# Kernel tuning notes

Hardware: AMD Instinct MI355X
Metric: run time of the kernel (lower is better)

## Reference

```python
import jax, jax.numpy as jnp
import numpy as np

B, C, E = 2, 128, 60000

def conv1(x, W, b):
    # pointwise conv1d: x [B,Cin,E], W [Cout,Cin], b [Cout] -> [B,Cout,E]
    return jnp.einsum('oc,bce->boe', W, x) + b[None, :, None]

def mesh_conv(x, gi, W, b):
    # MeshCNN GeMM conv: x [B,C,E], gi [B,E,4] neighbor edge ids, W [Cout,Cin,5], b [Cout]
    f = jax.vmap(lambda xb, ib: xb[:, ib])(x, gi)  # [B,C,E,4] neighbor gather
    f1, f2, f3, f4 = f[..., 0], f[..., 1], f[..., 2], f[..., 3]
    # symmetric features: [e, a+c, b+d, |a-c|, |b-d|]
    G = jnp.stack([x, f1 + f3, f2 + f4, jnp.abs(f1 - f3), jnp.abs(f2 - f4)], axis=-1)  # [B,C,E,5]
    return jnp.einsum('bces,ocs->boe', G, W) + b[None, :, None]


def setup_inputs() -> dict:
    key = jax.random.key(0)
    ks = jax.random.split(key, 16)
    s = 0.05
    return {
        'x_0': jax.random.normal(ks[0], (B, C, E), jnp.float32),
        'x_1': jax.random.normal(ks[1], (B, C, E), jnp.float32),
        'gemm': jax.random.randint(ks[2], (B, E, 4), 0, E, jnp.int32),
        'Wa_local': jax.random.normal(ks[3], (C, C), jnp.float32) * s,
        'ba_local': jax.random.normal(ks[4], (C,), jnp.float32) * s,
        'Wb_local': jax.random.normal(ks[5], (C, C), jnp.float32) * s,
        'bb_local': jax.random.normal(ks[6], (C,), jnp.float32) * s,
        'Wa_tri': jax.random.normal(ks[7], (C, C, 5), jnp.float32) * s,
        'ba_tri': jax.random.normal(ks[8], (C,), jnp.float32) * s,
        'Wb_tri': jax.random.normal(ks[9], (C, C, 5), jnp.float32) * s,
        'bb_tri': jax.random.normal(ks[10], (C,), jnp.float32) * s,
        'Wa_fuse': jax.random.normal(ks[11], (3, 2 * C), jnp.float32) * s,
        'ba_fuse': jax.random.normal(ks[12], (3,), jnp.float32) * s,
        'Wb_fuse': jax.random.normal(ks[13], (3, 2 * C), jnp.float32) * s,
        'bb_fuse': jax.random.normal(ks[14], (3,), jnp.float32) * s,
    }


def reference(x_0, x_1, gemm, Wa_local, ba_local, Wb_local, bb_local,
              Wa_tri, ba_tri, Wb_tri, bb_tri,
              Wa_fuse, ba_fuse, Wb_fuse, bb_fuse):
    a_local = conv1(x_0, Wa_local, ba_local)              # [B,C,E]
    a_tri = mesh_conv(x_0, gemm, Wa_tri, ba_tri)          # [B,C,E]
    x_a_two = jnp.concatenate([a_local, a_tri], axis=1)   # [B,2C,E]
    b_local = conv1(x_1, Wb_local, bb_local)
    b_tri = mesh_conv(x_1, gemm, Wb_tri, bb_tri)
    x_b_two = jnp.concatenate([b_local, b_tri], axis=1)
    x_a_w = conv1(x_a_two, Wa_fuse, ba_fuse)[:, None]     # [B,1,3,E]
    x_b_w = conv1(x_b_two, Wb_fuse, bb_fuse)[:, None]     # [B,1,3,E]
    return x_a_w + x_b_w
```

## Files before the change

### kernel.cpp

```cpp
#include <hip/hip_runtime.h>
#include <hip/hip_bf16.h>
#include <cstdint>

#define B_ 2
#define C_ 128
#define E_ 60000

typedef unsigned int uint32_;
typedef unsigned short ushort_;
typedef float v2f __attribute__((ext_vector_type(2)));

__device__ __forceinline__ v2f bp2(uint32_ v) {
    v2f r;
    r.x = __uint_as_float(v << 16);
    r.y = __uint_as_float(v & 0xffff0000u);
    return r;
}

__device__ __forceinline__ v2f vabs2(v2f a) {
    v2f r; r.x = fabsf(a.x); r.y = fabsf(a.y); return r;
}

__device__ __forceinline__ ushort_ f2b(float f) {
    union { float f; uint32_ u; } x; x.f = f;
    uint32_ u = x.u + 0x7fffu + ((x.u >> 16) & 1u);
    return (ushort_)(u >> 16);
}

__device__ __forceinline__ float swz_add(float v, const int pat) {
    switch (pat) {
    case 1:  return v + __int_as_float(__builtin_amdgcn_ds_swizzle(__float_as_int(v), 0x041F));
    case 2:  return v + __int_as_float(__builtin_amdgcn_ds_swizzle(__float_as_int(v), 0x081F));
    case 4:  return v + __int_as_float(__builtin_amdgcn_ds_swizzle(__float_as_int(v), 0x101F));
    case 8:  return v + __int_as_float(__builtin_amdgcn_ds_swizzle(__float_as_int(v), 0x201F));
    default: return v + __int_as_float(__builtin_amdgcn_ds_swizzle(__float_as_int(v), 0x401F));
    }
}

__global__ __launch_bounds__(256) void fuse_weights_kernel(
    const float* __restrict__ Wa_local, const float* __restrict__ ba_local,
    const float* __restrict__ Wb_local, const float* __restrict__ bb_local,
    const float* __restrict__ Wa_tri,  const float* __restrict__ ba_tri,
    const float* __restrict__ Wb_tri,  const float* __restrict__ bb_tri,
    const float* __restrict__ Wa_fuse, const float* __restrict__ ba_fuse,
    const float* __restrict__ Wb_fuse, const float* __restrict__ bb_fuse,
    float* __restrict__ Vw, float* __restrict__ cst)
{
    const int lane = threadIdx.x & 63;
    if (blockIdx.x < 15) {
        const int wid   = blockIdx.x * 4 + (threadIdx.x >> 6);
        const int pj    = wid / 10;
        const int chunk = wid % 10;
        const int p = pj / 3, j = pj % 3;
        const int f = chunk * 64 + lane;
        const float* Wf = p ? Wb_fuse : Wa_fuse;
        const float* Wt = p ? Wb_tri  : Wa_tri;
        const float* Wl = p ? Wb_local : Wa_local;
        float a0 = 0.f, a1 = 0.f, a2 = 0.f, a3 = 0.f;
        for (int o = 0; o < C_; o += 4) {
            a0 += Wf[j * 256 + 128 + o]     * Wt[(o)     * 640 + f];
            a1 += Wf[j * 256 + 128 + o + 1] * Wt[(o + 1) * 640 + f];
            a2 += Wf[j * 256 + 128 + o + 2] * Wt[(o + 2) * 640 + f];
            a3 += Wf[j * 256 + 128 + o + 3] * Wt[(o + 3) * 640 + f];
        }
        float acc = (a0 + a1) + (a2 + a3);
        const int s = f % 5, c = f / 5;
        if (s == 0) {
            float b0 = 0.f, b1 = 0.f, b2 = 0.f, b3 = 0.f;
            for (int o = 0; o < C_; o += 4) {
                b0 += Wf[j * 256 + o]     * Wl[(o)     * C_ + c];
                b1 += Wf[j * 256 + o + 1] * Wl[(o + 1) * C_ + c];
                b2 += Wf[j * 256 + o + 2] * Wl[(o + 2) * C_ + c];
                b3 += Wf[j * 256 + o + 3] * Wl[(o + 3) * C_ + c];
            }
            acc += (b0 + b1) + (b2 + b3);
        }
        Vw[(pj * 5 + s) * C_ + c] = acc;
    } else {
        if (threadIdx.x < 3) {
            int j = threadIdx.x;
            float acc = ba_fuse[j] + bb_fuse[j];
            for (int o = 0; o < C_; ++o) {
                acc += Wa_fuse[j * 256 + o]       * ba_local[o]
                     + Wa_fuse[j * 256 + 128 + o] * ba_tri[o]
                     + Wb_fuse[j * 256 + o]       * bb_local[o]
                     + Wb_fuse[j * 256 + 128 + o] * bb_tri[o];
            }
            cst[j] = acc;
        }
    }
}

__global__ __launch_bounds__(256) void transpose_bf16_kernel(
    const float* __restrict__ x0, const float* __restrict__ x1,
    ushort_* __restrict__ x0t, ushort_* __restrict__ x1t)
{
    __shared__ float tile[32][65];
    const int which = blockIdx.z >> 1;
    const int b     = blockIdx.z & 1;
    const float* src = (which ? x1 : x0) + (size_t)b * C_ * E_;
    ushort_*     dst = (which ? x1t : x0t) + (size_t)b * E_ * C_;
    const int e0 = blockIdx.x * 32;
    const int c0 = blockIdx.y * 64;
    const int t  = threadIdx.x;
    {
        const int c  = t >> 2;
        const int e8 = (t & 3) * 8;
        const float* p = src + (size_t)(c0 + c) * E_ + e0 + e8;
        float4 v0 = *(const float4*)p;
        float4 v1 = *(const float4*)(p + 4);
        tile[e8 + 0][c] = v0.x; tile[e8 + 1][c] = v0.y;
        tile[e8 + 2][c] = v0.z; tile[e8 + 3][c] = v0.w;
        tile[e8 + 4][c] = v1.x; tile[e8 + 5][c] = v1.y;
        tile[e8 + 6][c] = v1.z; tile[e8 + 7][c] = v1.w;
    }
    __syncthreads();
    {
        const int e  = t >> 3;
        const int c8 = (t & 7) * 8;
        const float* r = &tile[e][c8];
        uint32_ w0 = (uint32_)f2b(r[0]) | ((uint32_)f2b(r[1]) << 16);
        uint32_ w1 = (uint32_)f2b(r[2]) | ((uint32_)f2b(r[3]) << 16);
        uint32_ w2 = (uint32_)f2b(r[4]) | ((uint32_)f2b(r[5]) << 16);
        uint32_ w3 = (uint32_)f2b(r[6]) | ((uint32_)f2b(r[7]) << 16);
        uint4 w; w.x = w0; w.y = w1; w.z = w2; w.w = w3;
        *(uint4*)(dst + (size_t)(e0 + e) * C_ + c0 + c8) = w;
    }
}

__global__ __launch_bounds__(256, 4) void mesh_fused_kernel(
    const uint32_* __restrict__ x0t, const uint32_* __restrict__ x1t,
    const int* __restrict__ gemm, const float* __restrict__ Vw,
    const float* __restrict__ cst, float* __restrict__ out)
{
    const int lane = threadIdx.x & 63;
    const int wv   = threadIdx.x >> 6;
    const int gw   = blockIdx.x * 4 + wv;
    const int nw   = gridDim.x * 4;

    v2f w[2][3][5];
#pragma unroll
    for (int p = 0; p < 2; ++p)
#pragma unroll
        for (int j = 0; j < 3; ++j)
#pragma unroll
            for (int s = 0; s < 5; ++s)
                w[p][j][s] = *(const v2f*)(Vw + (((p * 3 + j) * 5 + s) << 7) + lane * 2);

    const int  jj     = lane >> 4;
    const bool is0    = (jj == 0), is1 = (jj == 1);
    const bool writer = ((lane & 15) == 0) && (jj < 3);
    const float cj    = is0 ? cst[0] : (is1 ? cst[1] : cst[2]);
    float* obase      = out + (size_t)(jj < 3 ? jj : 2) * E_;

    const int4* g4 = (const int4*)gemm;
    const int npair = (B_ * E_) / 2;

    int4 giA = make_int4(0, 0, 0, 0), giB = giA;
    if (gw < npair) { giA = g4[2 * gw]; giB = g4[2 * gw + 1]; }

    for (int pair = gw; pair < npair; pair += nw) {
        const int nxt = pair + nw;
        const int4 gA = giA, gB = giB;
        if (nxt < npair) { giA = g4[2 * nxt]; giB = g4[2 * nxt + 1]; }

        const int e0 = 2 * pair;
        const int b  = (e0 >= E_) ? 1 : 0;
        const int e  = e0 - (b ? E_ : 0);
        const uint32_* xa = x0t + (size_t)b * (E_ * 64);
        const uint32_* xb = x1t + (size_t)b * (E_ * 64);

        const uint32_ sA = ((uint32_)e << 6) + lane;
        const uint32_ sB = sA + 64;
        const uint32_ oA1 = ((uint32_)gA.x << 6) + lane;
        const uint32_ oA2 = ((uint32_)gA.y << 6) + lane;
        const uint32_ oA3 = ((uint32_)gA.z << 6) + lane;
        const uint32_ oA4 = ((uint32_)gA.w << 6) + lane;
        const uint32_ oB1 = ((uint32_)gB.x << 6) + lane;
        const uint32_ oB2 = ((uint32_)gB.y << 6) + lane;
        const uint32_ oB3 = ((uint32_)gB.z << 6) + lane;
        const uint32_ oB4 = ((uint32_)gB.w << 6) + lane;

        const uint32_ A0 = xa[sA],  A1 = xa[oA1], A2 = xa[oA2], A3 = xa[oA3], A4 = xa[oA4];
        const uint32_ C0 = xb[sA],  C1 = xb[oA1], C2 = xb[oA2], C3 = xb[oA3], C4 = xb[oA4];
        const uint32_ D0 = xa[sB],  D1 = xa[oB1], D2 = xa[oB2], D3 = xa[oB3], D4 = xa[oB4];
        const uint32_ F0 = xb[sB],  F1 = xb[oB1], F2 = xb[oB2], F3 = xb[oB3], F4 = xb[oB4];

        float rA0, rA1, rA2;
        {
            v2f a0 = bp2(A0), a1 = bp2(A1), a2 = bp2(A2), a3 = bp2(A3), a4 = bp2(A4);
            v2f b0 = bp2(C0), b1 = bp2(C1), b2 = bp2(C2), b3 = bp2(C3), b4 = bp2(C4);
            v2f sa1 = a1 + a3, sa2 = a2 + a4;
            v2f da1 = vabs2(a1 - a3), da2 = vabs2(a2 - a4);
            v2f sb1 = b1 + b3, sb2 = b2 + b4;
            v2f db1 = vabs2(b1 - b3), db2 = vabs2(b2 - b4);
            v2f t0 = w[0][0][0] * a0, t1 = w[0][1][0] * a0, t2 = w[0][2][0] * a0;
            t0 += w[0][0][1] * sa1; t1 += w[0][1][1] * sa1; t2 += w[0][2][1] * sa1;
            t0 += w[0][0][2] * sa2; t1 += w[0][1][2] * sa2; t2 += w[0][2][2] * sa2;
            t0 += w[0][0][3] * da1; t1 += w[0][1][3] * da1; t2 += w[0][2][3] * da1;
            t0 += w[0][0][4] * da2; t1 += w[0][1][4] * da2; t2 += w[0][2][4] * da2;
            t0 += w[1][0][0] * b0;  t1 += w[1][1][0] * b0;  t2 += w[1][2][0] * b0;
            t0 += w[1][0][1] * sb1; t1 += w[1][1][1] * sb1; t2 += w[1][2][1] * sb1;
            t0 += w[1][0][2] * sb2; t1 += w[1][1][2] * sb2; t2 += w[1][2][2] * sb2;
            t0 += w[1][0][3] * db1; t1 += w[1][1][3] * db1; t2 += w[1][2][3] * db1;
            t0 += w[1][0][4] * db2; t1 += w[1][1][4] * db2; t2 += w[1][2][4] * db2;
            rA0 = t0.x + t0.y; rA1 = t1.x + t1.y; rA2 = t2.x + t2.y;
        }
        float rB0, rB1, rB2;
        {
            v2f a0 = bp2(D0), a1 = bp2(D1), a2 = bp2(D2), a3 = bp2(D3), a4 = bp2(D4);
            v2f b0 = bp2(F0), b1 = bp2(F1), b2 = bp2(F2), b3 = bp2(F3), b4 = bp2(F4);
            v2f sa1 = a1 + a3, sa2 = a2 + a4;
            v2f da1 = vabs2(a1 - a3), da2 = vabs2(a2 - a4);
            v2f sb1 = b1 + b3, sb2 = b2 + b4;
            v2f db1 = vabs2(b1 - b3), db2 = vabs2(b2 - b4);
            v2f t0 = w[0][0][0] * a0, t1 = w[0][1][0] * a0, t2 = w[0][2][0] * a0;
            t0 += w[0][0][1] * sa1; t1 += w[0][1][1] * sa1; t2 += w[0][2][1] * sa1;
            t0 += w[0][0][2] * sa2; t1 += w[0][1][2] * sa2; t2 += w[0][2][2] * sa2;
            t0 += w[0][0][3] * da1; t1 += w[0][1][3] * da1; t2 += w[0][2][3] * da1;
            t0 += w[0][0][4] * da2; t1 += w[0][1][4] * da2; t2 += w[0][2][4] * da2;
            t0 += w[1][0][0] * b0;  t1 += w[1][1][0] * b0;  t2 += w[1][2][0] * b0;
            t0 += w[1][0][1] * sb1; t1 += w[1][1][1] * sb1; t2 += w[1][2][1] * sb1;
            t0 += w[1][0][2] * sb2; t1 += w[1][1][2] * sb2; t2 += w[1][2][2] * sb2;
            t0 += w[1][0][3] * db1; t1 += w[1][1][3] * db1; t2 += w[1][2][3] * db1;
            t0 += w[1][0][4] * db2; t1 += w[1][1][4] * db2; t2 += w[1][2][4] * db2;
            rB0 = t0.x + t0.y; rB1 = t1.x + t1.y; rB2 = t2.x + t2.y;
        }

        rA0 = swz_add(rA0, 16); rB0 = swz_add(rB0, 16);
        rA1 = swz_add(rA1, 16); rB1 = swz_add(rB1, 16);
        rA2 = swz_add(rA2, 16); rB2 = swz_add(rB2, 16);
        rA0 += __shfl_xor(rA0, 32, 64); rB0 += __shfl_xor(rB0, 32, 64);
        rA1 += __shfl_xor(rA1, 32, 64); rB1 += __shfl_xor(rB1, 32, 64);
        rA2 += __shfl_xor(rA2, 32, 64); rB2 += __shfl_xor(rB2, 32, 64);

        float vA = is0 ? rA0 : (is1 ? rA1 : rA2);
        float vB = is0 ? rB0 : (is1 ? rB1 : rB2);
        vA = swz_add(vA, 1); vB = swz_add(vB, 1);
        vA = swz_add(vA, 2); vB = swz_add(vB, 2);
        vA = swz_add(vA, 4); vB = swz_add(vB, 4);
        vA = swz_add(vA, 8); vB = swz_add(vB, 8);

        if (writer) {
            float2 st; st.x = vA + cj; st.y = vB + cj;
            *(float2*)(obase + (b ? 3 * E_ : 0) + e) = st;
        }
    }
}

extern "C" void kernel_launch(void* const* d_in, const int* in_sizes, int n_in,
                              void* d_out, int out_size, void* d_ws, size_t ws_size,
                              hipStream_t stream) {
    const float* x0       = (const float*)d_in[0];
    const float* x1       = (const float*)d_in[1];
    const int*   gemm     = (const int*)d_in[2];
    const float* Wa_local = (const float*)d_in[3];
    const float* ba_local = (const float*)d_in[4];
    const float* Wb_local = (const float*)d_in[5];
    const float* bb_local = (const float*)d_in[6];
    const float* Wa_tri   = (const float*)d_in[7];
    const float* ba_tri   = (const float*)d_in[8];
    const float* Wb_tri   = (const float*)d_in[9];
    const float* bb_tri   = (const float*)d_in[10];
    const float* Wa_fuse  = (const float*)d_in[11];
    const float* ba_fuse  = (const float*)d_in[12];
    const float* Wb_fuse  = (const float*)d_in[13];
    const float* bb_fuse  = (const float*)d_in[14];
    float* out = (float*)d_out;

    ushort_* x0t = (ushort_*)d_ws;
    ushort_* x1t = x0t + (size_t)B_ * E_ * C_;
    float*   Vw  = (float*)(x1t + (size_t)B_ * E_ * C_);
    float*   cst = Vw + 2 * 3 * 5 * C_;

    hipLaunchKernelGGL(fuse_weights_kernel, dim3(16), dim3(256), 0, stream,
                       Wa_local, ba_local, Wb_local, bb_local,
                       Wa_tri, ba_tri, Wb_tri, bb_tri,
                       Wa_fuse, ba_fuse, Wb_fuse, bb_fuse, Vw, cst);

    hipLaunchKernelGGL(transpose_bf16_kernel, dim3(E_ / 32, C_ / 64, 2 * B_),
                       dim3(256), 0, stream, x0, x1, x0t, x1t);

    hipLaunchKernelGGL(mesh_fused_kernel, dim3(2048), dim3(256), 0, stream,
                       (const uint32_*)x0t, (const uint32_*)x1t, gemm, Vw, cst, out);
}
```

Measured before the change: 225.3 us.

## Merge prep kernels, interleave x0/x1 rows, software-pipeline gathers in mesh kernel

Folds the weight-fusion and transpose kernels into one launch, parallelising the weight reduction across warps and computing the bias constants with a wave reduction. The transposed bf16 activations of x0 and x1 are interleaved per edge so each neighbour fetch touches one contiguous 512-byte record. The main gather loop is software-pipelined so the next pair's gathers are issued before the current pair is computed. Holding a second set of gathered values raises register pressure, so occupancy is lowered to 3 blocks per CU.

```diff
diff --git a/kernel.cpp b/kernel.cpp
--- a/kernel.cpp
+++ b/kernel.cpp
@@ -37,37 +37,41 @@
     }
 }
 
-__global__ __launch_bounds__(256) void fuse_weights_kernel(
+__global__ __launch_bounds__(256) void prep_kernel(
+    const float* __restrict__ x0, const float* __restrict__ x1,
     const float* __restrict__ Wa_local, const float* __restrict__ ba_local,
     const float* __restrict__ Wb_local, const float* __restrict__ bb_local,
     const float* __restrict__ Wa_tri,  const float* __restrict__ ba_tri,
     const float* __restrict__ Wb_tri,  const float* __restrict__ bb_tri,
     const float* __restrict__ Wa_fuse, const float* __restrict__ ba_fuse,
     const float* __restrict__ Wb_fuse, const float* __restrict__ bb_fuse,
-    float* __restrict__ Vw, float* __restrict__ cst)
+    ushort_* __restrict__ xt, float* __restrict__ Vw, float* __restrict__ cst)
 {
+    __shared__ float smem[32 * 65];
     const int lane = threadIdx.x & 63;
-    if (blockIdx.x < 15) {
-        const int wid   = blockIdx.x * 4 + (threadIdx.x >> 6);
-        const int pj    = wid / 10;
-        const int chunk = wid % 10;
+    const int wv   = threadIdx.x >> 6;
+
+    if (blockIdx.x < 60) {
+        const int pj    = blockIdx.x / 10;
+        const int chunk = blockIdx.x % 10;
         const int p = pj / 3, j = pj % 3;
         const int f = chunk * 64 + lane;
         const float* Wf = p ? Wb_fuse : Wa_fuse;
         const float* Wt = p ? Wb_tri  : Wa_tri;
         const float* Wl = p ? Wb_local : Wa_local;
+        const int o0 = wv * 32;
         float a0 = 0.f, a1 = 0.f, a2 = 0.f, a3 = 0.f;
-        for (int o = 0; o < C_; o += 4) {
+        for (int o = o0; o < o0 + 32; o += 4) {
             a0 += Wf[j * 256 + 128 + o]     * Wt[(o)     * 640 + f];
-            a1 += Wf[j * 256 + 128 + o + 1] * Wt[(o + 1) * 640 + f];
-            a2 += Wf[j * 256 + 128 + o + 2] * Wt[(o + 2) * 640 + f];
-            a3 += Wf[j * 256 + 128 + o + 3] * Wt[(o + 3) * 640 + f];
+            a1 += Wf[j * 256 + 129 + o]     * Wt[(o + 1) * 640 + f];
+            a2 += Wf[j * 256 + 130 + o]     * Wt[(o + 2) * 640 + f];
+            a3 += Wf[j * 256 + 131 + o]     * Wt[(o + 3) * 640 + f];
         }
         float acc = (a0 + a1) + (a2 + a3);
         const int s = f % 5, c = f / 5;
         if (s == 0) {
             float b0 = 0.f, b1 = 0.f, b2 = 0.f, b3 = 0.f;
-            for (int o = 0; o < C_; o += 4) {
+            for (int o = o0; o < o0 + 32; o += 4) {
                 b0 += Wf[j * 256 + o]     * Wl[(o)     * C_ + c];
                 b1 += Wf[j * 256 + o + 1] * Wl[(o + 1) * C_ + c];
                 b2 += Wf[j * 256 + o + 2] * Wl[(o + 2) * C_ + c];
@@ -75,63 +79,139 @@
             }
             acc += (b0 + b1) + (b2 + b3);
         }
-        Vw[(pj * 5 + s) * C_ + c] = acc;
+        smem[wv * 64 + lane] = acc;
+        __syncthreads();
+        if (wv == 0) {
+            float tot = smem[lane] + smem[64 + lane] + smem[128 + lane] + smem[192 + lane];
+            Vw[(pj * 5 + s) * C_ + c] = tot;
+        }
+    } else if (blockIdx.x == 60) {
+        const int j = wv;
+        if (j < 3) {
+            float acc;
+            {
+                const int l = lane;
+                acc = Wa_fuse[j * 256 + l]       * ba_local[l]
+                    + Wa_fuse[j * 256 + 128 + l] * ba_tri[l]
+                    + Wb_fuse[j * 256 + l]       * bb_local[l]
+                    + Wb_fuse[j * 256 + 128 + l] * bb_tri[l];
+            }
+            {
+                const int l = lane + 64;
+                acc += Wa_fuse[j * 256 + l]       * ba_local[l]
+                     + Wa_fuse[j * 256 + 128 + l] * ba_tri[l]
+                     + Wb_fuse[j * 256 + l]       * bb_local[l]
+                     + Wb_fuse[j * 256 + 128 + l] * bb_tri[l];
+            }
+            acc = swz_add(acc, 1); acc = swz_add(acc, 2); acc = swz_add(acc, 4);
+            acc = swz_add(acc, 8); acc = swz_add(acc, 16);
+            acc += __shfl_xor(acc, 32, 64);
+            if (lane == 0) cst[j] = acc + ba_fuse[j] + bb_fuse[j];
+        }
     } else {
-        if (threadIdx.x < 3) {
-            int j = threadIdx.x;
-            float acc = ba_fuse[j] + bb_fuse[j];
-            for (int o = 0; o < C_; ++o) {
-                acc += Wa_fuse[j * 256 + o]       * ba_local[o]
-                     + Wa_fuse[j * 256 + 128 + o] * ba_tri[o]
-                     + Wb_fuse[j * 256 + o]       * bb_local[o]
-                     + Wb_fuse[j * 256 + 128 + o] * bb_tri[o];
-            }
-            cst[j] = acc;
+        const int tb = blockIdx.x - 61;
+        const int bx = tb % 1875;
+        const int rz = tb / 1875;
+        const int by = rz & 1;
+        const int bz = rz >> 1;
+        const int which = bz >> 1;
+        const int b     = bz & 1;
+        const float* src = (which ? x1 : x0) + (size_t)b * C_ * E_;
+        const int e0 = bx * 32;
+        const int c0 = by * 64;
+        const int t  = threadIdx.x;
+        float (*tile)[65] = (float(*)[65])smem;
+        {
+            const int c  = t >> 2;
+            const int e8 = (t & 3) * 8;
+            const float* pp = src + (size_t)(c0 + c) * E_ + e0 + e8;
+            float4 v0 = *(const float4*)pp;
+            float4 v1 = *(const float4*)(pp + 4);
+            tile[e8 + 0][c] = v0.x; tile[e8 + 1][c] = v0.y;
+            tile[e8 + 2][c] = v0.z; tile[e8 + 3][c] = v0.w;
+            tile[e8 + 4][c] = v1.x; tile[e8 + 5][c] = v1.y;
+            tile[e8 + 6][c] = v1.z; tile[e8 + 7][c] = v1.w;
+        }
+        __syncthreads();
+        {
+            const int e  = t >> 3;
+            const int c8 = (t & 7) * 8;
+            const float* r = &tile[e][c8];
+            uint32_ w0 = (uint32_)f2b(r[0]) | ((uint32_)f2b(r[1]) << 16);
+            uint32_ w1 = (uint32_)f2b(r[2]) | ((uint32_)f2b(r[3]) << 16);
+            uint32_ w2 = (uint32_)f2b(r[4]) | ((uint32_)f2b(r[5]) << 16);
+            uint32_ w3 = (uint32_)f2b(r[6]) | ((uint32_)f2b(r[7]) << 16);
+            uint4 w; w.x = w0; w.y = w1; w.z = w2; w.w = w3;
+            const size_t rec = (size_t)((b * E_ + e0 + e) * 2 + which);
+            *(uint4*)(xt + (rec << 7) + c0 + c8) = w;
         }
     }
 }
 
-__global__ __launch_bounds__(256) void transpose_bf16_kernel(
-    const float* __restrict__ x0, const float* __restrict__ x1,
-    ushort_* __restrict__ x0t, ushort_* __restrict__ x1t)
+struct GD {
+    uint32_ A0, A1, A2, A3, A4;
+    uint32_ Cc0, Cc1, Cc2, Cc3, Cc4;
+    uint32_ D0, D1, D2, D3, D4;
+    uint32_ F0, F1, F2, F3, F4;
+};
+
+__device__ __forceinline__ GD issue_loads(const uint32_* __restrict__ xt,
+                                          int pair, int4 gA, int4 gB, int lane)
 {
-    __shared__ float tile[32][65];
-    const int which = blockIdx.z >> 1;
-    const int b     = blockIdx.z & 1;
-    const float* src = (which ? x1 : x0) + (size_t)b * C_ * E_;
-    ushort_*     dst = (which ? x1t : x0t) + (size_t)b * E_ * C_;
-    const int e0 = blockIdx.x * 32;
-    const int c0 = blockIdx.y * 64;
-    const int t  = threadIdx.x;
-    {
-        const int c  = t >> 2;
-        const int e8 = (t & 3) * 8;
-        const float* p = src + (size_t)(c0 + c) * E_ + e0 + e8;
-        float4 v0 = *(const float4*)p;
-        float4 v1 = *(const float4*)(p + 4);
-        tile[e8 + 0][c] = v0.x; tile[e8 + 1][c] = v0.y;
-        tile[e8 + 2][c] = v0.z; tile[e8 + 3][c] = v0.w;
-        tile[e8 + 4][c] = v1.x; tile[e8 + 5][c] = v1.y;
-        tile[e8 + 6][c] = v1.z; tile[e8 + 7][c] = v1.w;
-    }
-    __syncthreads();
-    {
-        const int e  = t >> 3;
-        const int c8 = (t & 7) * 8;
-        const float* r = &tile[e][c8];
-        uint32_ w0 = (uint32_)f2b(r[0]) | ((uint32_)f2b(r[1]) << 16);
-        uint32_ w1 = (uint32_)f2b(r[2]) | ((uint32_)f2b(r[3]) << 16);
-        uint32_ w2 = (uint32_)f2b(r[4]) | ((uint32_)f2b(r[5]) << 16);
-        uint32_ w3 = (uint32_)f2b(r[6]) | ((uint32_)f2b(r[7]) << 16);
-        uint4 w; w.x = w0; w.y = w1; w.z = w2; w.w = w3;
-        *(uint4*)(dst + (size_t)(e0 + e) * C_ + c0 + c8) = w;
-    }
-}
-
-__global__ __launch_bounds__(256, 4) void mesh_fused_kernel(
-    const uint32_* __restrict__ x0t, const uint32_* __restrict__ x1t,
-    const int* __restrict__ gemm, const float* __restrict__ Vw,
-    const float* __restrict__ cst, float* __restrict__ out)
+    const int e0 = 2 * pair;
+    const uint32_ badd = (e0 >= E_) ? (uint32_)E_ : 0u;
+    const uint32_ sA = ((uint32_)e0 << 7) + lane;
+    const uint32_ sB = sA + 128;
+    const uint32_ n1 = ((badd + (uint32_)gA.x) << 7) + lane;
+    const uint32_ n2 = ((badd + (uint32_)gA.y) << 7) + lane;
+    const uint32_ n3 = ((badd + (uint32_)gA.z) << 7) + lane;
+    const uint32_ n4 = ((badd + (uint32_)gA.w) << 7) + lane;
+    const uint32_ m1 = ((badd + (uint32_)gB.x) << 7) + lane;
+    const uint32_ m2 = ((badd + (uint32_)gB.y) << 7) + lane;
+    const uint32_ m3 = ((badd + (uint32_)gB.z) << 7) + lane;
+    const uint32_ m4 = ((badd + (uint32_)gB.w) << 7) + lane;
+    GD g;
+    g.A0 = xt[sA]; g.Cc0 = xt[sA + 64];
+    g.A1 = xt[n1]; g.Cc1 = xt[n1 + 64];
+    g.A2 = xt[n2]; g.Cc2 = xt[n2 + 64];
+    g.A3 = xt[n3]; g.Cc3 = xt[n3 + 64];
+    g.A4 = xt[n4]; g.Cc4 = xt[n4 + 64];
+    g.D0 = xt[sB]; g.F0 = xt[sB + 64];
+    g.D1 = xt[m1]; g.F1 = xt[m1 + 64];
+    g.D2 = xt[m2]; g.F2 = xt[m2 + 64];
+    g.D3 = xt[m3]; g.F3 = xt[m3 + 64];
+    g.D4 = xt[m4]; g.F4 = xt[m4 + 64];
+    return g;
+}
+
+__device__ __forceinline__ void edge3(uint32_ X0, uint32_ X1, uint32_ X2, uint32_ X3, uint32_ X4,
+                                      uint32_ Y0, uint32_ Y1, uint32_ Y2, uint32_ Y3, uint32_ Y4,
+                                      const v2f (*w)[3][5],
+                                      float& r0, float& r1, float& r2)
+{
+    v2f a0 = bp2(X0), a1 = bp2(X1), a2 = bp2(X2), a3 = bp2(X3), a4 = bp2(X4);
+    v2f b0 = bp2(Y0), b1 = bp2(Y1), b2 = bp2(Y2), b3 = bp2(Y3), b4 = bp2(Y4);
+    v2f sa1 = a1 + a3, sa2 = a2 + a4;
+    v2f da1 = vabs2(a1 - a3), da2 = vabs2(a2 - a4);
+    v2f sb1 = b1 + b3, sb2 = b2 + b4;
+    v2f db1 = vabs2(b1 - b3), db2 = vabs2(b2 - b4);
+    v2f t0 = w[0][0][0] * a0, t1 = w[0][1][0] * a0, t2 = w[0][2][0] * a0;
+    t0 += w[0][0][1] * sa1; t1 += w[0][1][1] * sa1; t2 += w[0][2][1] * sa1;
+    t0 += w[0][0][2] * sa2; t1 += w[0][1][2] * sa2; t2 += w[0][2][2] * sa2;
+    t0 += w[0][0][3] * da1; t1 += w[0][1][3] * da1; t2 += w[0][2][3] * da1;
+    t0 += w[0][0][4] * da2; t1 += w[0][1][4] * da2; t2 += w[0][2][4] * da2;
+    t0 += w[1][0][0] * b0;  t1 += w[1][1][0] * b0;  t2 += w[1][2][0] * b0;
+    t0 += w[1][0][1] * sb1; t1 += w[1][1][1] * sb1; t2 += w[1][2][1] * sb1;
+    t0 += w[1][0][2] * sb2; t1 += w[1][1][2] * sb2; t2 += w[1][2][2] * sb2;
+    t0 += w[1][0][3] * db1; t1 += w[1][1][3] * db1; t2 += w[1][2][3] * db1;
+    t0 += w[1][0][4] * db2; t1 += w[1][1][4] * db2; t2 += w[1][2][4] * db2;
+    r0 = t0.x + t0.y; r1 = t1.x + t1.y; r2 = t2.x + t2.y;
+}
+
+__global__ __launch_bounds__(256, 3) void mesh_fused_kernel(
+    const uint32_* __restrict__ xt, const int* __restrict__ gemm,
+    const float* __restrict__ Vw, const float* __restrict__ cst,
+    float* __restrict__ out)
 {
     const int lane = threadIdx.x & 63;
     const int wv   = threadIdx.x >> 6;
@@ -156,76 +236,22 @@
     const int4* g4 = (const int4*)gemm;
     const int npair = (B_ * E_) / 2;
 
-    int4 giA = make_int4(0, 0, 0, 0), giB = giA;
-    if (gw < npair) { giA = g4[2 * gw]; giB = g4[2 * gw + 1]; }
-
+    int pnext = (gw + nw < npair) ? gw + nw : gw;
+    int4 giA = g4[2 * gw], giB = g4[2 * gw + 1];
+    GD cur = issue_loads(xt, gw, giA, giB, lane);
+    int4 niA = g4[2 * pnext], niB = g4[2 * pnext + 1];
+
+#pragma unroll 2
     for (int pair = gw; pair < npair; pair += nw) {
-        const int nxt = pair + nw;
-        const int4 gA = giA, gB = giB;
-        if (nxt < npair) { giA = g4[2 * nxt]; giB = g4[2 * nxt + 1]; }
-
-        const int e0 = 2 * pair;
-        const int b  = (e0 >= E_) ? 1 : 0;
-        const int e  = e0 - (b ? E_ : 0);
-        const uint32_* xa = x0t + (size_t)b * (E_ * 64);
-        const uint32_* xb = x1t + (size_t)b * (E_ * 64);
-
-        const uint32_ sA = ((uint32_)e << 6) + lane;
-        const uint32_ sB = sA + 64;
-        const uint32_ oA1 = ((uint32_)gA.x << 6) + lane;
-        const uint32_ oA2 = ((uint32_)gA.y << 6) + lane;
-        const uint32_ oA3 = ((uint32_)gA.z << 6) + lane;
-        const uint32_ oA4 = ((uint32_)gA.w << 6) + lane;
-        const uint32_ oB1 = ((uint32_)gB.x << 6) + lane;
-        const uint32_ oB2 = ((uint32_)gB.y << 6) + lane;
-        const uint32_ oB3 = ((uint32_)gB.z << 6) + lane;
-        const uint32_ oB4 = ((uint32_)gB.w << 6) + lane;
-
-        const uint32_ A0 = xa[sA],  A1 = xa[oA1], A2 = xa[oA2], A3 = xa[oA3], A4 = xa[oA4];
-        const uint32_ C0 = xb[sA],  C1 = xb[oA1], C2 = xb[oA2], C3 = xb[oA3], C4 = xb[oA4];
-        const uint32_ D0 = xa[sB],  D1 = xa[oB1], D2 = xa[oB2], D3 = xa[oB3], D4 = xa[oB4];
-        const uint32_ F0 = xb[sB],  F1 = xb[oB1], F2 = xb[oB2], F3 = xb[oB3], F4 = xb[oB4];
-
-        float rA0, rA1, rA2;
-        {
-            v2f a0 = bp2(A0), a1 = bp2(A1), a2 = bp2(A2), a3 = bp2(A3), a4 = bp2(A4);
-            v2f b0 = bp2(C0), b1 = bp2(C1), b2 = bp2(C2), b3 = bp2(C3), b4 = bp2(C4);
-            v2f sa1 = a1 + a3, sa2 = a2 + a4;
-            v2f da1 = vabs2(a1 - a3), da2 = vabs2(a2 - a4);
-            v2f sb1 = b1 + b3, sb2 = b2 + b4;
-            v2f db1 = vabs2(b1 - b3), db2 = vabs2(b2 - b4);
-            v2f t0 = w[0][0][0] * a0, t1 = w[0][1][0] * a0, t2 = w[0][2][0] * a0;
-            t0 += w[0][0][1] * sa1; t1 += w[0][1][1] * sa1; t2 += w[0][2][1] * sa1;
-            t0 += w[0][0][2] * sa2; t1 += w[0][1][2] * sa2; t2 += w[0][2][2] * sa2;
-            t0 += w[0][0][3] * da1; t1 += w[0][1][3] * da1; t2 += w[0][2][3] * da1;
-            t0 += w[0][0][4] * da2; t1 += w[0][1][4] * da2; t2 += w[0][2][4] * da2;
-            t0 += w[1][0][0] * b0;  t1 += w[1][1][0] * b0;  t2 += w[1][2][0] * b0;
-            t0 += w[1][0][1] * sb1; t1 += w[1][1][1] * sb1; t2 += w[1][2][1] * sb1;
-            t0 += w[1][0][2] * sb2; t1 += w[1][1][2] * sb2; t2 += w[1][2][2] * sb2;
-            t0 += w[1][0][3] * db1; t1 += w[1][1][3] * db1; t2 += w[1][2][3] * db1;
-            t0 += w[1][0][4] * db2; t1 += w[1][1][4] * db2; t2 += w[1][2][4] * db2;
-            rA0 = t0.x + t0.y; rA1 = t1.x + t1.y; rA2 = t2.x + t2.y;
-        }
-        float rB0, rB1, rB2;
-        {
-            v2f a0 = bp2(D0), a1 = bp2(D1), a2 = bp2(D2), a3 = bp2(D3), a4 = bp2(D4);
-            v2f b0 = bp2(F0), b1 = bp2(F1), b2 = bp2(F2), b3 = bp2(F3), b4 = bp2(F4);
-            v2f sa1 = a1 + a3, sa2 = a2 + a4;
-            v2f da1 = vabs2(a1 - a3), da2 = vabs2(a2 - a4);
-            v2f sb1 = b1 + b3, sb2 = b2 + b4;
-            v2f db1 = vabs2(b1 - b3), db2 = vabs2(b2 - b4);
-            v2f t0 = w[0][0][0] * a0, t1 = w[0][1][0] * a0, t2 = w[0][2][0] * a0;
-            t0 += w[0][0][1] * sa1; t1 += w[0][1][1] * sa1; t2 += w[0][2][1] * sa1;
-            t0 += w[0][0][2] * sa2; t1 += w[0][1][2] * sa2; t2 += w[0][2][2] * sa2;
-            t0 += w[0][0][3] * da1; t1 += w[0][1][3] * da1; t2 += w[0][2][3] * da1;
-            t0 += w[0][0][4] * da2; t1 += w[0][1][4] * da2; t2 += w[0][2][4] * da2;
-            t0 += w[1][0][0] * b0;  t1 += w[1][1][0] * b0;  t2 += w[1][2][0] * b0;
-            t0 += w[1][0][1] * sb1; t1 += w[1][1][1] * sb1; t2 += w[1][2][1] * sb1;
-            t0 += w[1][0][2] * sb2; t1 += w[1][1][2] * sb2; t2 += w[1][2][2] * sb2;
-            t0 += w[1][0][3] * db1; t1 += w[1][1][3] * db1; t2 += w[1][2][3] * db1;
-            t0 += w[1][0][4] * db2; t1 += w[1][1][4] * db2; t2 += w[1][2][4] * db2;
-            rB0 = t0.x + t0.y; rB1 = t1.x + t1.y; rB2 = t2.x + t2.y;
-        }
+        GD nb = issue_loads(xt, pnext, niA, niB, lane);
+        const int p2 = (pnext + nw < npair) ? pnext + nw : pnext;
+        niA = g4[2 * p2]; niB = g4[2 * p2 + 1];
+
+        float rA0, rA1, rA2, rB0, rB1, rB2;
+        edge3(cur.A0, cur.A1, cur.A2, cur.A3, cur.A4,
+              cur.Cc0, cur.Cc1, cur.Cc2, cur.Cc3, cur.Cc4, w, rA0, rA1, rA2);
+        edge3(cur.D0, cur.D1, cur.D2, cur.D3, cur.D4,
+              cur.F0, cur.F1, cur.F2, cur.F3, cur.F4, w, rB0, rB1, rB2);
 
         rA0 = swz_add(rA0, 16); rB0 = swz_add(rB0, 16);
         rA1 = swz_add(rA1, 16); rB1 = swz_add(rB1, 16);
@@ -242,9 +268,15 @@
         vA = swz_add(vA, 8); vB = swz_add(vB, 8);
 
         if (writer) {
+            const int e0p = 2 * pair;
+            const int bb  = (e0p >= E_) ? 1 : 0;
+            const int ee  = e0p - (bb ? E_ : 0);
             float2 st; st.x = vA + cj; st.y = vB + cj;
-            *(float2*)(obase + (b ? 3 * E_ : 0) + e) = st;
-        }
+            *(float2*)(obase + (bb ? 3 * E_ : 0) + ee) = st;
+        }
+
+        cur = nb;
+        pnext = p2;
     }
 }
 
@@ -268,19 +300,16 @@
     const float* bb_fuse  = (const float*)d_in[14];
     float* out = (float*)d_out;
 
-    ushort_* x0t = (ushort_*)d_ws;
-    ushort_* x1t = x0t + (size_t)B_ * E_ * C_;
-    float*   Vw  = (float*)(x1t + (size_t)B_ * E_ * C_);
+    ushort_* xt  = (ushort_*)d_ws;
+    float*   Vw  = (float*)(xt + (size_t)B_ * E_ * 2 * C_);
     float*   cst = Vw + 2 * 3 * 5 * C_;
 
-    hipLaunchKernelGGL(fuse_weights_kernel, dim3(16), dim3(256), 0, stream,
+    hipLaunchKernelGGL(prep_kernel, dim3(61 + 15000), dim3(256), 0, stream,
+                       x0, x1,
                        Wa_local, ba_local, Wb_local, bb_local,
                        Wa_tri, ba_tri, Wb_tri, bb_tri,
-                       Wa_fuse, ba_fuse, Wb_fuse, bb_fuse, Vw, cst);
-
-    hipLaunchKernelGGL(transpose_bf16_kernel, dim3(E_ / 32, C_ / 64, 2 * B_),
-                       dim3(256), 0, stream, x0, x1, x0t, x1t);
+                       Wa_fuse, ba_fuse, Wb_fuse, bb_fuse, xt, Vw, cst);
 
     hipLaunchKernelGGL(mesh_fused_kernel, dim3(2048), dim3(256), 0, stream,
-                       (const uint32_*)x0t, (const uint32_*)x1t, gemm, Vw, cst, out);
-}
+                       (const uint32_*)xt, gemm, Vw, cst, out);
+}
```

Result: faster. 214.8 us (-4.6%).
